# Performance work log

Hardware: AMD Instinct MI355X
Metric: run time of the kernel (lower is better)

Reference implementation:

```python
import jax, jax.numpy as jnp
import numpy as np

B, CH, H, W = 1, 128, 160, 224


def _lrelu(x):
    return jax.nn.leaky_relu(x, 0.01)


def _conv(x, w, b):
    # 1x1 conv: x [B,Cin,H,W], w [Cout,Cin], b [Cout]
    return jnp.einsum('bchw,oc->bohw', x, w) + b[None, :, None, None]


def _cmul(x, inds, Wt, b):
    # CondMul: x [N,Cin], inds [N] int32, Wt [classes,Cin,Cout], b [classes,Cout]
    return jnp.einsum('ni,nio->no', x, jnp.take(Wt, inds, axis=0)) + jnp.take(b, inds, axis=0)


def _forward(x_in, bb1_w, bb1_b, bb2_w, bb2_b, bb3_w, bb3_b,
             msk1_w, msk1_b, msk2_w, msk2_b, msk3_w, msk3_b,
             c10_w, c10_b, c20_w, c20_b, c30_w, c30_b,
             c11_W, c11_b, c21_W, c21_b, c31_W, c31_b,
             c12_W, c12_b, c22_W, c22_b, c32_W, c32_b,
             r1_w, r1_b, r2_W, r2_b, r3_W, r3_b):
    Bb, C, Hh, Ww = x_in.shape
    # backbone (1x1 convs)
    x = _lrelu(_conv(x_in, bb1_w, bb1_b))
    x = _lrelu(_conv(x, bb2_w, bb2_b))
    feat = _lrelu(_conv(x, bb3_w, bb3_b))  # [B,128,H,W]
    # mask head (note: torch applies leaky_relu to msk3 output too)
    m = _lrelu(_conv(x_in, msk1_w, msk1_b))
    m = _lrelu(_conv(m, msk2_w, msk2_b))
    mask = _lrelu(_conv(m, msk3_w, msk3_b))  # [B,1,H,W]
    # stage 1: dense classification over classes[0]=16
    y = _lrelu(_conv(feat, c10_w, c10_b))
    y = _lrelu(_conv(y, c20_w, c20_b))
    y = _conv(y, c30_w, c30_b)  # [B,16,H,W], no relu
    inds1 = jnp.argmax(y, axis=1).reshape(-1).astype(jnp.int32)  # [N], (b,h,w) order
    x_l = jnp.transpose(feat, (0, 2, 3, 1)).reshape(-1, feat.shape[1])  # [N,128]
    # stage 2: CondMul routed by inds1 (16 classes), out = 16+2*8 = 32
    t = _lrelu(_cmul(x_l, inds1, c11_W, c11_b))
    t = _lrelu(_cmul(t, inds1, c21_W, c21_b))
    t = _cmul(t, inds1, c31_W, c31_b)
    inds2 = jnp.argmax(t, axis=1).astype(jnp.int32)
    inds12 = jnp.clip(inds1 * 16 + (inds2 - 8), 0, 255).astype(jnp.int32)
    # stage 3: CondMul routed by inds12 (256 classes)
    t = _lrelu(_cmul(x_l, inds12, c12_W, c12_b))
    t = _lrelu(_cmul(t, inds12, c22_W, c22_b))
    t = _cmul(t, inds12, c32_W, c32_b)
    inds3 = jnp.argmax(t, axis=1).astype(jnp.int32)
    inds123 = jnp.clip(inds12 * 16 + (inds3 - 8), 0, 4095).astype(jnp.int32)  # classes123-1
    inds_super = inds123 // 512  # class_factor = 4096/8
    xr = _lrelu(_conv(x_in, r1_w, r1_b))
    xr_l = jnp.transpose(xr, (0, 2, 3, 1)).reshape(-1, xr.shape[1])  # [N,128]
    t = _lrelu(_cmul(xr_l, inds_super, r2_W, r2_b))
    r = _cmul(t, inds123, r3_W, r3_b).reshape(-1)
    out = ((inds123.astype(jnp.float32) + r) * (1.0 / 4096.0)).reshape(Bb, 1, Hh, Ww)
    return out, mask


def setup_inputs():
    ks = jax.random.split(jax.random.key(0), 40)
    ctr = iter(range(40))

    def p(shape, scale=0.05):
        return jax.random.normal(ks[next(ctr)], shape, dtype=jnp.float32) * scale

    d = {
        'x_in': p((B, CH, H, W), 1.0),
        'bb1_w': p((128, 128)), 'bb1_b': p((128,)),
        'bb2_w': p((128, 128)), 'bb2_b': p((128,)),
        'bb3_w': p((128, 128)), 'bb3_b': p((128,)),
        'msk1_w': p((32, 128)), 'msk1_b': p((32,)),
        'msk2_w': p((16, 32)), 'msk2_b': p((16,)),
        'msk3_w': p((1, 16)), 'msk3_b': p((1,)),
        'c10_w': p((32, 128)), 'c10_b': p((32,)),
        'c20_w': p((32, 32)), 'c20_b': p((32,)),
        'c30_w': p((16, 32)), 'c30_b': p((16,)),
        'c11_W': p((16, 128, 32)), 'c11_b': p((16, 32)),
        'c21_W': p((16, 32, 32)), 'c21_b': p((16, 32)),
        'c31_W': p((16, 32, 32)), 'c31_b': p((16, 32)),
        'c12_W': p((256, 128, 32)), 'c12_b': p((256, 32)),
        'c22_W': p((256, 32, 32)), 'c22_b': p((256, 32)),
        'c32_W': p((256, 32, 32)), 'c32_b': p((256, 32)),
        'r1_w': p((128, 128)), 'r1_b': p((128,)),
        'r2_W': p((8, 128, 32)), 'r2_b': p((8, 32)),
        'r3_W': p((4096, 32, 1)), 'r3_b': p((4096, 1)),
    }
    return d


def reference(x_in, bb1_w, bb1_b, bb2_w, bb2_b, bb3_w, bb3_b,
              msk1_w, msk1_b, msk2_w, msk2_b, msk3_w, msk3_b,
              c10_w, c10_b, c20_w, c20_b, c30_w, c30_b,
              c11_W, c11_b, c21_W, c21_b, c31_W, c31_b,
              c12_W, c12_b, c22_W, c22_b, c32_W, c32_b,
              r1_w, r1_b, r2_W, r2_b, r3_W, r3_b):
    return _forward(x_in, bb1_w, bb1_b, bb2_w, bb2_b, bb3_w, bb3_b,
                    msk1_w, msk1_b, msk2_w, msk2_b, msk3_w, msk3_b,
                    c10_w, c10_b, c20_w, c20_b, c30_w, c30_b,
                    c11_W, c11_b, c21_W, c21_b, c31_W, c31_b,
                    c12_W, c12_b, c22_W, c22_b, c32_W, c32_b,
                    r1_w, r1_b, r2_W, r2_b, r3_W, r3_b)
```

## Files before the change

### kernel.cpp

```cpp
#include <hip/hip_runtime.h>

#define N_PIX (160*224)
#define ORDER_CAP (396*256)
#define CHUNK_CAP 512
#define G_S2 156
#define G_S3 396
#define G_RG 148
#define NB   70
#define BCHUNK 512

__device__ __forceinline__ float lrelu(float v) { return v >= 0.f ? v : 0.01f * v; }

template<int CHW>
__global__ __launch_bounds__(256) void dense128_k(const float* __restrict__ in,
    const float* __restrict__ W, const float* __restrict__ b,
    float* __restrict__ out, int N)
{
  __shared__ float Wl[128*128];
  const int tid = threadIdx.x;
#pragma unroll
  for (int k = 0; k < 16; ++k)
    ((float4*)Wl)[k*256 + tid] = ((const float4*)W)[k*256 + tid];
  const int lane = tid & 63;
  const int t = tid >> 6;
  const int p = blockIdx.x * 64 + lane;
  float acc[32];
#pragma unroll
  for (int o = 0; o < 32; ++o) acc[o] = b[t*32 + o];
  __syncthreads();
  const float* xin = CHW ? (in + p) : (in + (size_t)p * 128);
  for (int c0 = 0; c0 < 128; c0 += 8) {
    float xs[8];
    if (CHW) {
#pragma unroll
      for (int k = 0; k < 8; ++k) xs[k] = xin[(size_t)(c0 + k) * N];
    } else {
      float4 xa = *(const float4*)(xin + c0);
      float4 xb = *(const float4*)(xin + c0 + 4);
      xs[0]=xa.x; xs[1]=xa.y; xs[2]=xa.z; xs[3]=xa.w;
      xs[4]=xb.x; xs[5]=xb.y; xs[6]=xb.z; xs[7]=xb.w;
    }
#pragma unroll
    for (int o = 0; o < 32; ++o) {
      const float* wr = &Wl[(t*32 + o)*128 + c0];
      float4 w0 = *(const float4*)wr;
      float4 w1 = *(const float4*)(wr + 4);
      acc[o] += xs[0]*w0.x + xs[1]*w0.y + xs[2]*w0.z + xs[3]*w0.w
              + xs[4]*w1.x + xs[5]*w1.y + xs[6]*w1.z + xs[7]*w1.w;
    }
  }
  __syncthreads();
  float4* orow = (float4*)(out + (size_t)p * 128 + t*32);
#pragma unroll
  for (int o4 = 0; o4 < 8; ++o4)
    orow[o4] = make_float4(lrelu(acc[4*o4+0]), lrelu(acc[4*o4+1]),
                           lrelu(acc[4*o4+2]), lrelu(acc[4*o4+3]));
}

__global__ __launch_bounds__(256) void mask_k(const float* __restrict__ xg,
    const float* __restrict__ W1, const float* __restrict__ b1,
    const float* __restrict__ W2, const float* __restrict__ b2,
    const float* __restrict__ W3, const float* __restrict__ b3,
    float* __restrict__ outm, int N)
{
  __shared__ float W1l[32*128], W2l[16*32], W3l[16];
  const int tid = threadIdx.x;
#pragma unroll
  for (int k = 0; k < 4; ++k)
    ((float4*)W1l)[k*256 + tid] = ((const float4*)W1)[k*256 + tid];
  if (tid < 128) ((float4*)W2l)[tid] = ((const float4*)W2)[tid];
  if (tid < 4)   ((float4*)W3l)[tid] = ((const float4*)W3)[tid];
  __syncthreads();
  const int p = blockIdx.x * 256 + tid;
  float a1[32];
#pragma unroll
  for (int o = 0; o < 32; ++o) a1[o] = b1[o];
  for (int c0 = 0; c0 < 128; c0 += 8) {
    float xs[8];
#pragma unroll
    for (int k = 0; k < 8; ++k) xs[k] = xg[(size_t)(c0 + k) * N + p];
#pragma unroll
    for (int o = 0; o < 32; ++o) {
      const float* wr = &W1l[o*128 + c0];
      float4 w0 = *(const float4*)wr, w1 = *(const float4*)(wr + 4);
      a1[o] += xs[0]*w0.x + xs[1]*w0.y + xs[2]*w0.z + xs[3]*w0.w
             + xs[4]*w1.x + xs[5]*w1.y + xs[6]*w1.z + xs[7]*w1.w;
    }
  }
#pragma unroll
  for (int o = 0; o < 32; ++o) a1[o] = lrelu(a1[o]);
  float a2[16];
#pragma unroll
  for (int o = 0; o < 16; ++o) a2[o] = b2[o];
#pragma unroll
  for (int i = 0; i < 32; i += 4) {
#pragma unroll
    for (int o = 0; o < 16; ++o) {
      float4 w = *(const float4*)&W2l[o*32 + i];
      a2[o] += a1[i]*w.x + a1[i+1]*w.y + a1[i+2]*w.z + a1[i+3]*w.w;
    }
  }
#pragma unroll
  for (int o = 0; o < 16; ++o) a2[o] = lrelu(a2[o]);
  float a3 = b3[0];
#pragma unroll
  for (int i = 0; i < 16; i += 4) {
    float4 w = *(const float4*)&W3l[i];
    a3 += a2[i]*w.x + a2[i+1]*w.y + a2[i+2]*w.z + a2[i+3]*w.w;
  }
  outm[p] = lrelu(a3);
}

__global__ __launch_bounds__(256) void stage1_k(const float* __restrict__ feat,
    const float* __restrict__ W1, const float* __restrict__ b1,
    const float* __restrict__ W2, const float* __restrict__ b2,
    const float* __restrict__ W3, const float* __restrict__ b3,
    int* __restrict__ inds1, int N)
{
  __shared__ float W1l[32*128], W2l[32*32], W3l[16*32];
  const int tid = threadIdx.x;
#pragma unroll
  for (int k = 0; k < 4; ++k)
    ((float4*)W1l)[k*256 + tid] = ((const float4*)W1)[k*256 + tid];
  ((float4*)W2l)[tid] = ((const float4*)W2)[tid];
  if (tid < 128) ((float4*)W3l)[tid] = ((const float4*)W3)[tid];
  __syncthreads();
  const int p = blockIdx.x * 256 + tid;
  const float* x = feat + (size_t)p * 128;
  float a1[32];
#pragma unroll
  for (int o = 0; o < 32; ++o) a1[o] = b1[o];
  for (int c0 = 0; c0 < 128; c0 += 8) {
    float4 xa = *(const float4*)(x + c0);
    float4 xb = *(const float4*)(x + c0 + 4);
    float xs[8] = {xa.x, xa.y, xa.z, xa.w, xb.x, xb.y, xb.z, xb.w};
#pragma unroll
    for (int o = 0; o < 32; ++o) {
      const float* wr = &W1l[o*128 + c0];
      float4 w0 = *(const float4*)wr, w1 = *(const float4*)(wr + 4);
      a1[o] += xs[0]*w0.x + xs[1]*w0.y + xs[2]*w0.z + xs[3]*w0.w
             + xs[4]*w1.x + xs[5]*w1.y + xs[6]*w1.z + xs[7]*w1.w;
    }
  }
#pragma unroll
  for (int o = 0; o < 32; ++o) a1[o] = lrelu(a1[o]);
  float a2[32];
#pragma unroll
  for (int o = 0; o < 32; ++o) a2[o] = b2[o];
#pragma unroll
  for (int i = 0; i < 32; i += 4) {
#pragma unroll
    for (int o = 0; o < 32; ++o) {
      float4 w = *(const float4*)&W2l[o*32 + i];
      a2[o] += a1[i]*w.x + a1[i+1]*w.y + a1[i+2]*w.z + a1[i+3]*w.w;
    }
  }
#pragma unroll
  for (int o = 0; o < 32; ++o) a2[o] = lrelu(a2[o]);
  float lg[16];
#pragma unroll
  for (int o = 0; o < 16; ++o) lg[o] = b3[o];
#pragma unroll
  for (int i = 0; i < 32; i += 4) {
#pragma unroll
    for (int o = 0; o < 16; ++o) {
      float4 w = *(const float4*)&W3l[o*32 + i];
      lg[o] += a2[i]*w.x + a2[i+1]*w.y + a2[i+2]*w.z + a2[i+3]*w.w;
    }
  }
  float bv = lg[0]; int bi = 0;
#pragma unroll
  for (int o = 1; o < 16; ++o) if (lg[o] > bv) { bv = lg[o]; bi = o; }
  inds1[p] = bi;
}

__global__ __launch_bounds__(256) void stage23_k(const float* __restrict__ act,
    const float* __restrict__ W1g, const float* __restrict__ b1g,
    const float* __restrict__ W2g, const float* __restrict__ b2g,
    const float* __restrict__ W3g, const float* __restrict__ b3g,
    const int* __restrict__ chunk_class, const int* __restrict__ order,
    const int* __restrict__ offs_this, const int* __restrict__ cnts_this,
    int* __restrict__ out_ind, int hi)
{
  const int cls = chunk_class[blockIdx.x];
  if (cls < 0) return;
  __shared__ float W1l[128*32], W2l[32*32], W3l[32*32];
  __shared__ float b1l[32], b2l[32], b3l[32];
  const int tid = threadIdx.x;
  const float* W1 = W1g + (size_t)cls * 4096;
  const float* W2 = W2g + (size_t)cls * 1024;
  const float* W3 = W3g + (size_t)cls * 1024;
#pragma unroll
  for (int k = 0; k < 4; ++k)
    ((float4*)W1l)[k*256 + tid] = ((const float4*)W1)[k*256 + tid];
  ((float4*)W2l)[tid] = ((const float4*)W2)[tid];
  ((float4*)W3l)[tid] = ((const float4*)W3)[tid];
  if (tid < 32) {
    b1l[tid] = b1g[cls*32 + tid];
    b2l[tid] = b2g[cls*32 + tid];
    b3l[tid] = b3g[cls*32 + tid];
  }
  const int slot = blockIdx.x * 256 + tid;
  const int end = offs_this[cls] + cnts_this[cls];
  __syncthreads();
  if (slot >= end) return;
  const int p = order[slot];
  const float* x = act + (size_t)p * 128;
  float a1[32];
#pragma unroll
  for (int o = 0; o < 32; ++o) a1[o] = b1l[o];
  for (int i0 = 0; i0 < 128; i0 += 8) {
    float4 xa = *(const float4*)(x + i0);
    float4 xb = *(const float4*)(x + i0 + 4);
    float xs[8] = {xa.x, xa.y, xa.z, xa.w, xb.x, xb.y, xb.z, xb.w};
#pragma unroll
    for (int i = 0; i < 8; ++i) {
#pragma unroll
      for (int o4 = 0; o4 < 8; ++o4) {
        float4 w = *(const float4*)&W1l[(i0 + i)*32 + o4*4];
        a1[o4*4+0] += xs[i]*w.x; a1[o4*4+1] += xs[i]*w.y;
        a1[o4*4+2] += xs[i]*w.z; a1[o4*4+3] += xs[i]*w.w;
      }
    }
  }
#pragma unroll
  for (int o = 0; o < 32; ++o) a1[o] = lrelu(a1[o]);
  float a2[32];
#pragma unroll
  for (int o = 0; o < 32; ++o) a2[o] = b2l[o];
#pragma unroll
  for (int i = 0; i < 32; ++i) {
#pragma unroll
    for (int o4 = 0; o4 < 8; ++o4) {
      float4 w = *(const float4*)&W2l[i*32 + o4*4];
      a2[o4*4+0] += a1[i]*w.x; a2[o4*4+1] += a1[i]*w.y;
      a2[o4*4+2] += a1[i]*w.z; a2[o4*4+3] += a1[i]*w.w;
    }
  }
#pragma unroll
  for (int o = 0; o < 32; ++o) a2[o] = lrelu(a2[o]);
  float a3[32];
#pragma unroll
  for (int o = 0; o < 32; ++o) a3[o] = b3l[o];
#pragma unroll
  for (int i = 0; i < 32; ++i) {
#pragma unroll
    for (int o4 = 0; o4 < 8; ++o4) {
      float4 w = *(const float4*)&W3l[i*32 + o4*4];
      a3[o4*4+0] += a2[i]*w.x; a3[o4*4+1] += a2[i]*w.y;
      a3[o4*4+2] += a2[i]*w.z; a3[o4*4+3] += a2[i]*w.w;
    }
  }
  float bv = a3[0]; int bi = 0;
#pragma unroll
  for (int o = 1; o < 32; ++o) if (a3[o] > bv) { bv = a3[o]; bi = o; }
  int v = cls*16 + bi - 8;
  v = v < 0 ? 0 : (v > hi ? hi : v);
  out_ind[p] = v;
}

__global__ __launch_bounds__(256) void reg_k(const float* __restrict__ act,
    const float* __restrict__ W1g, const float* __restrict__ b1g,
    const float* __restrict__ r3W, const float* __restrict__ r3b,
    const int* __restrict__ chunk_class, const int* __restrict__ order,
    const int* __restrict__ offs_this, const int* __restrict__ cnts_this,
    const int* __restrict__ inds123, float* __restrict__ outr)
{
  const int cls = chunk_class[blockIdx.x];
  if (cls < 0) return;
  __shared__ float W1l[128*32], b1l[32];
  const int tid = threadIdx.x;
  const float* W1 = W1g + (size_t)cls * 4096;
#pragma unroll
  for (int k = 0; k < 4; ++k)
    ((float4*)W1l)[k*256 + tid] = ((const float4*)W1)[k*256 + tid];
  if (tid < 32) b1l[tid] = b1g[cls*32 + tid];
  const int slot = blockIdx.x * 256 + tid;
  const int end = offs_this[cls] + cnts_this[cls];
  __syncthreads();
  if (slot >= end) return;
  const int p = order[slot];
  const float* x = act + (size_t)p * 128;
  float a1[32];
#pragma unroll
  for (int o = 0; o < 32; ++o) a1[o] = b1l[o];
  for (int i0 = 0; i0 < 128; i0 += 8) {
    float4 xa = *(const float4*)(x + i0);
    float4 xb = *(const float4*)(x + i0 + 4);
    float xs[8] = {xa.x, xa.y, xa.z, xa.w, xb.x, xb.y, xb.z, xb.w};
#pragma unroll
    for (int i = 0; i < 8; ++i) {
#pragma unroll
      for (int o4 = 0; o4 < 8; ++o4) {
        float4 w = *(const float4*)&W1l[(i0 + i)*32 + o4*4];
        a1[o4*4+0] += xs[i]*w.x; a1[o4*4+1] += xs[i]*w.y;
        a1[o4*4+2] += xs[i]*w.z; a1[o4*4+3] += xs[i]*w.w;
      }
    }
  }
#pragma unroll
  for (int o = 0; o < 32; ++o) a1[o] = lrelu(a1[o]);
  const int ind = inds123[p];
  const float4* rw = (const float4*)(r3W + (size_t)ind * 32);
  float r = r3b[ind];
#pragma unroll
  for (int k = 0; k < 8; ++k) {
    float4 w = rw[k];
    r += a1[4*k+0]*w.x + a1[4*k+1]*w.y + a1[4*k+2]*w.z + a1[4*k+3]*w.w;
  }
  outr[p] = ((float)ind + r) * (1.0f / 4096.0f);
}

__global__ __launch_bounds__(256) void hist_k(const int* __restrict__ ind,
    int* __restrict__ blkcnt, int shift, int C)
{
  __shared__ int h[256];
  const int tid = threadIdx.x, b = blockIdx.x;
  h[tid] = 0;
  __syncthreads();
  const int base = b * BCHUNK;
  atomicAdd(&h[ind[base + tid] >> shift], 1);
  atomicAdd(&h[ind[base + 256 + tid] >> shift], 1);
  __syncthreads();
  if (tid < C) blkcnt[b * C + tid] = h[tid];
}

__global__ __launch_bounds__(256) void scan_k(const int* __restrict__ blkcnt,
    int* __restrict__ blkbase, int* __restrict__ offsets, int* __restrict__ counts,
    int* __restrict__ chunk_class, int C, int fillTo)
{
  __shared__ int cl[256], ol[256];
  __shared__ int totChunks;
  const int tid = threadIdx.x;
  if (tid < C) {
    int s = 0;
    for (int b = 0; b < NB; ++b) s += blkcnt[b * C + tid];
    cl[tid] = s;
  }
  __syncthreads();
  if (tid == 0) {
    int off = 0;
    for (int c = 0; c < C; ++c) {
      ol[c] = off;
      off += ((cl[c] + 255) >> 8) << 8;
    }
    totChunks = off >> 8;
  }
  __syncthreads();
  if (tid < C) {
    offsets[tid] = ol[tid];
    counts[tid]  = cl[tid];
    int acc = ol[tid];
    for (int b = 0; b < NB; ++b) {
      int v = blkcnt[b * C + tid];
      blkbase[b * C + tid] = acc;
      acc += v;
    }
    const int start = ol[tid] >> 8;
    const int nch = (cl[tid] + 255) >> 8;
    for (int k = 0; k < nch; ++k) chunk_class[start + k] = tid;
  }
  for (int k = totChunks + tid; k < fillTo; k += 256) chunk_class[k] = -1;
}

__global__ __launch_bounds__(256) void scatter_k(const int* __restrict__ ind,
    const int* __restrict__ blkbase, int* __restrict__ order, int shift, int C)
{
  __shared__ int lcur[256], lbase[256];
  const int tid = threadIdx.x, b = blockIdx.x;
  lcur[tid] = 0;
  if (tid < C) lbase[tid] = blkbase[b * C + tid];
  __syncthreads();
  const int base = b * BCHUNK;
#pragma unroll
  for (int r = 0; r < BCHUNK; r += 256) {
    const int p = base + r + tid;
    const int c = ind[p] >> shift;
    const int rank = atomicAdd(&lcur[c], 1);
    order[lbase[c] + rank] = p;
  }
}

extern "C" void kernel_launch(void* const* d_in, const int* in_sizes, int n_in,
                              void* d_out, int out_size, void* d_ws, size_t ws_size,
                              hipStream_t stream)
{
  const int N = N_PIX;
  const float* x_in  = (const float*)d_in[0];
  const float* bb1_w = (const float*)d_in[1];  const float* bb1_b = (const float*)d_in[2];
  const float* bb2_w = (const float*)d_in[3];  const float* bb2_b = (const float*)d_in[4];
  const float* bb3_w = (const float*)d_in[5];  const float* bb3_b = (const float*)d_in[6];
  const float* msk1_w= (const float*)d_in[7];  const float* msk1_b= (const float*)d_in[8];
  const float* msk2_w= (const float*)d_in[9];  const float* msk2_b= (const float*)d_in[10];
  const float* msk3_w= (const float*)d_in[11]; const float* msk3_b= (const float*)d_in[12];
  const float* c10_w = (const float*)d_in[13]; const float* c10_b = (const float*)d_in[14];
  const float* c20_w = (const float*)d_in[15]; const float* c20_b = (const float*)d_in[16];
  const float* c30_w = (const float*)d_in[17]; const float* c30_b = (const float*)d_in[18];
  const float* c11_W = (const float*)d_in[19]; const float* c11_b = (const float*)d_in[20];
  const float* c21_W = (const float*)d_in[21]; const float* c21_b = (const float*)d_in[22];
  const float* c31_W = (const float*)d_in[23]; const float* c31_b = (const float*)d_in[24];
  const float* c12_W = (const float*)d_in[25]; const float* c12_b = (const float*)d_in[26];
  const float* c22_W = (const float*)d_in[27]; const float* c22_b = (const float*)d_in[28];
  const float* c32_W = (const float*)d_in[29]; const float* c32_b = (const float*)d_in[30];
  const float* r1_w  = (const float*)d_in[31]; const float* r1_b  = (const float*)d_in[32];
  const float* r2_W  = (const float*)d_in[33]; const float* r2_b  = (const float*)d_in[34];
  const float* r3_W  = (const float*)d_in[35]; const float* r3_b  = (const float*)d_in[36];

  float* act     = (float*)d_ws;
  int*   inds1   = (int*)(act + (size_t)N * 128);
  int*   inds12  = inds1 + N;
  int*   inds123 = inds12 + N;
  int*   counts  = inds123 + N;
  int*   offs    = counts + 256;
  int*   chunk_cls = offs + 256;
  int*   order     = chunk_cls + CHUNK_CAP;
  int*   blkcnt    = order + ORDER_CAP;
  int*   blkbase   = blkcnt + NB*256;

  float* out_reg  = (float*)d_out;
  float* out_mask = out_reg + N;

  const dim3 B(256);
  const int gPix64  = N / 64;
  const int gPix256 = N / 256;

  dense128_k<1><<<gPix64, B, 0, stream>>>(x_in, bb1_w, bb1_b, act, N);
  dense128_k<0><<<gPix64, B, 0, stream>>>(act,  bb2_w, bb2_b, act, N);
  dense128_k<0><<<gPix64, B, 0, stream>>>(act,  bb3_w, bb3_b, act, N);

  mask_k<<<gPix256, B, 0, stream>>>(x_in, msk1_w, msk1_b, msk2_w, msk2_b,
                                    msk3_w, msk3_b, out_mask, N);

  stage1_k<<<gPix256, B, 0, stream>>>(act, c10_w, c10_b, c20_w, c20_b,
                                      c30_w, c30_b, inds1, N);

  hist_k<<<NB, B, 0, stream>>>(inds1, blkcnt, 0, 16);
  scan_k<<<1, B, 0, stream>>>(blkcnt, blkbase, offs, counts, chunk_cls, 16, G_S2);
  scatter_k<<<NB, B, 0, stream>>>(inds1, blkbase, order, 0, 16);
  stage23_k<<<G_S2, B, 0, stream>>>(act, c11_W, c11_b, c21_W, c21_b, c31_W, c31_b,
                                    chunk_cls, order, offs, counts, inds12, 255);

  hist_k<<<NB, B, 0, stream>>>(inds12, blkcnt, 0, 256);
  scan_k<<<1, B, 0, stream>>>(blkcnt, blkbase, offs, counts, chunk_cls, 256, G_S3);
  scatter_k<<<NB, B, 0, stream>>>(inds12, blkbase, order, 0, 256);
  stage23_k<<<G_S3, B, 0, stream>>>(act, c12_W, c12_b, c22_W, c22_b, c32_W, c32_b,
                                    chunk_cls, order, offs, counts, inds123, 4095);

  dense128_k<1><<<gPix64, B, 0, stream>>>(x_in, r1_w, r1_b, act, N);

  hist_k<<<NB, B, 0, stream>>>(inds123, blkcnt, 9, 8);
  scan_k<<<1, B, 0, stream>>>(blkcnt, blkbase, offs, counts, chunk_cls, 8, G_RG);
  scatter_k<<<NB, B, 0, stream>>>(inds123, blkbase, order, 9, 8);
  reg_k<<<G_RG, B, 0, stream>>>(act, r2_W, r2_b, r3_W, r3_b,
                                chunk_cls, order, offs, counts, inds123, out_reg);
}
```

Baseline: 526.3 us.

## Retile dense128 to two pixels per thread and fuse stage-1 histogram

The dense 1x1 conv kernel now runs 512-thread blocks covering 128 pixels. Each thread computes 16 outputs for two pixels, so every shared-memory weight load is reused twice and the LDS traffic per FMA is halved. Separately, stage1 builds the per-block class histogram with shared atomics and writes blkcnt directly. This removes one hist_k launch and its re-read of inds1. Scan and scatter take a block count and chunk size so they can consume the 140 blocks of 256 pixels, at the cost of extra atomics in stage1.

After: 533.4 us. Within noise of the previous version (+1.3%).

```diff
diff --git a/kernel.cpp b/kernel.cpp
--- a/kernel.cpp
+++ b/kernel.cpp
@@ -12,49 +12,63 @@
 __device__ __forceinline__ float lrelu(float v) { return v >= 0.f ? v : 0.01f * v; }
 
 template<int CHW>
-__global__ __launch_bounds__(256) void dense128_k(const float* __restrict__ in,
+__global__ __launch_bounds__(512) void dense128_k(const float* __restrict__ in,
     const float* __restrict__ W, const float* __restrict__ b,
     float* __restrict__ out, int N)
 {
   __shared__ float Wl[128*128];
   const int tid = threadIdx.x;
 #pragma unroll
-  for (int k = 0; k < 16; ++k)
-    ((float4*)Wl)[k*256 + tid] = ((const float4*)W)[k*256 + tid];
+  for (int k = 0; k < 8; ++k)
+    ((float4*)Wl)[k*512 + tid] = ((const float4*)W)[k*512 + tid];
   const int lane = tid & 63;
-  const int t = tid >> 6;
-  const int p = blockIdx.x * 64 + lane;
-  float acc[32];
-#pragma unroll
-  for (int o = 0; o < 32; ++o) acc[o] = b[t*32 + o];
-  __syncthreads();
-  const float* xin = CHW ? (in + p) : (in + (size_t)p * 128);
+  const int wv = tid >> 6;
+  const int ob = wv * 16;
+  const int p0 = blockIdx.x * 128 + lane;
+  const int p1 = p0 + 64;
+  float acc0[16], acc1[16];
+#pragma unroll
+  for (int o = 0; o < 16; ++o) { acc0[o] = b[ob + o]; acc1[o] = acc0[o]; }
+  __syncthreads();
+  const float* x0 = CHW ? (in + p0) : (in + (size_t)p0 * 128);
+  const float* x1 = CHW ? (in + p1) : (in + (size_t)p1 * 128);
   for (int c0 = 0; c0 < 128; c0 += 8) {
-    float xs[8];
+    float xa[8], xb[8];
     if (CHW) {
 #pragma unroll
-      for (int k = 0; k < 8; ++k) xs[k] = xin[(size_t)(c0 + k) * N];
+      for (int k = 0; k < 8; ++k) {
+        xa[k] = x0[(size_t)(c0 + k) * N];
+        xb[k] = x1[(size_t)(c0 + k) * N];
+      }
     } else {
-      float4 xa = *(const float4*)(xin + c0);
-      float4 xb = *(const float4*)(xin + c0 + 4);
-      xs[0]=xa.x; xs[1]=xa.y; xs[2]=xa.z; xs[3]=xa.w;
-      xs[4]=xb.x; xs[5]=xb.y; xs[6]=xb.z; xs[7]=xb.w;
-    }
-#pragma unroll
-    for (int o = 0; o < 32; ++o) {
-      const float* wr = &Wl[(t*32 + o)*128 + c0];
+      float4 a0 = *(const float4*)(x0 + c0), a1 = *(const float4*)(x0 + c0 + 4);
+      float4 b0 = *(const float4*)(x1 + c0), b1 = *(const float4*)(x1 + c0 + 4);
+      xa[0]=a0.x; xa[1]=a0.y; xa[2]=a0.z; xa[3]=a0.w;
+      xa[4]=a1.x; xa[5]=a1.y; xa[6]=a1.z; xa[7]=a1.w;
+      xb[0]=b0.x; xb[1]=b0.y; xb[2]=b0.z; xb[3]=b0.w;
+      xb[4]=b1.x; xb[5]=b1.y; xb[6]=b1.z; xb[7]=b1.w;
+    }
+#pragma unroll
+    for (int o = 0; o < 16; ++o) {
+      const float* wr = &Wl[(ob + o)*128 + c0];
       float4 w0 = *(const float4*)wr;
       float4 w1 = *(const float4*)(wr + 4);
-      acc[o] += xs[0]*w0.x + xs[1]*w0.y + xs[2]*w0.z + xs[3]*w0.w
-              + xs[4]*w1.x + xs[5]*w1.y + xs[6]*w1.z + xs[7]*w1.w;
-    }
-  }
-  __syncthreads();
-  float4* orow = (float4*)(out + (size_t)p * 128 + t*32);
-#pragma unroll
-  for (int o4 = 0; o4 < 8; ++o4)
-    orow[o4] = make_float4(lrelu(acc[4*o4+0]), lrelu(acc[4*o4+1]),
-                           lrelu(acc[4*o4+2]), lrelu(acc[4*o4+3]));
+      acc0[o] += xa[0]*w0.x + xa[1]*w0.y + xa[2]*w0.z + xa[3]*w0.w
+               + xa[4]*w1.x + xa[5]*w1.y + xa[6]*w1.z + xa[7]*w1.w;
+      acc1[o] += xb[0]*w0.x + xb[1]*w0.y + xb[2]*w0.z + xb[3]*w0.w
+               + xb[4]*w1.x + xb[5]*w1.y + xb[6]*w1.z + xb[7]*w1.w;
+    }
+  }
+  __syncthreads();
+  float4* o0 = (float4*)(out + (size_t)p0 * 128 + ob);
+  float4* o1 = (float4*)(out + (size_t)p1 * 128 + ob);
+#pragma unroll
+  for (int q = 0; q < 4; ++q) {
+    o0[q] = make_float4(lrelu(acc0[4*q+0]), lrelu(acc0[4*q+1]),
+                        lrelu(acc0[4*q+2]), lrelu(acc0[4*q+3]));
+    o1[q] = make_float4(lrelu(acc1[4*q+0]), lrelu(acc1[4*q+1]),
+                        lrelu(acc1[4*q+2]), lrelu(acc1[4*q+3]));
+  }
 }
 
 __global__ __launch_bounds__(256) void mask_k(const float* __restrict__ xg,
@@ -115,15 +129,17 @@
     const float* __restrict__ W1, const float* __restrict__ b1,
     const float* __restrict__ W2, const float* __restrict__ b2,
     const float* __restrict__ W3, const float* __restrict__ b3,
-    int* __restrict__ inds1, int N)
+    int* __restrict__ inds1, int* __restrict__ blkcnt, int N)
 {
   __shared__ float W1l[32*128], W2l[32*32], W3l[16*32];
+  __shared__ int hist[16];
   const int tid = threadIdx.x;
 #pragma unroll
   for (int k = 0; k < 4; ++k)
     ((float4*)W1l)[k*256 + tid] = ((const float4*)W1)[k*256 + tid];
   ((float4*)W2l)[tid] = ((const float4*)W2)[tid];
   if (tid < 128) ((float4*)W3l)[tid] = ((const float4*)W3)[tid];
+  if (tid < 16) hist[tid] = 0;
   __syncthreads();
   const int p = blockIdx.x * 256 + tid;
   const float* x = feat + (size_t)p * 128;
@@ -172,6 +188,9 @@
 #pragma unroll
   for (int o = 1; o < 16; ++o) if (lg[o] > bv) { bv = lg[o]; bi = o; }
   inds1[p] = bi;
+  atomicAdd(&hist[bi], 1);
+  __syncthreads();
+  if (tid < 16) blkcnt[blockIdx.x * 16 + tid] = hist[tid];
 }
 
 __global__ __launch_bounds__(256) void stage23_k(const float* __restrict__ act,
@@ -327,14 +346,14 @@
 
 __global__ __launch_bounds__(256) void scan_k(const int* __restrict__ blkcnt,
     int* __restrict__ blkbase, int* __restrict__ offsets, int* __restrict__ counts,
-    int* __restrict__ chunk_class, int C, int fillTo)
+    int* __restrict__ chunk_class, int C, int fillTo, int nb)
 {
   __shared__ int cl[256], ol[256];
   __shared__ int totChunks;
   const int tid = threadIdx.x;
   if (tid < C) {
     int s = 0;
-    for (int b = 0; b < NB; ++b) s += blkcnt[b * C + tid];
+    for (int b = 0; b < nb; ++b) s += blkcnt[b * C + tid];
     cl[tid] = s;
   }
   __syncthreads();
@@ -351,7 +370,7 @@
     offsets[tid] = ol[tid];
     counts[tid]  = cl[tid];
     int acc = ol[tid];
-    for (int b = 0; b < NB; ++b) {
+    for (int b = 0; b < nb; ++b) {
       int v = blkcnt[b * C + tid];
       blkbase[b * C + tid] = acc;
       acc += v;
@@ -364,16 +383,16 @@
 }
 
 __global__ __launch_bounds__(256) void scatter_k(const int* __restrict__ ind,
-    const int* __restrict__ blkbase, int* __restrict__ order, int shift, int C)
+    const int* __restrict__ blkbase, int* __restrict__ order, int shift, int C,
+    int chunkpx)
 {
   __shared__ int lcur[256], lbase[256];
   const int tid = threadIdx.x, b = blockIdx.x;
   lcur[tid] = 0;
   if (tid < C) lbase[tid] = blkbase[b * C + tid];
   __syncthreads();
-  const int base = b * BCHUNK;
-#pragma unroll
-  for (int r = 0; r < BCHUNK; r += 256) {
+  const int base = b * chunkpx;
+  for (int r = 0; r < chunkpx; r += 256) {
     const int p = base + r + tid;
     const int c = ind[p] >> shift;
     const int rank = atomicAdd(&lcur[c], 1);
@@ -415,42 +434,42 @@
   int*   chunk_cls = offs + 256;
   int*   order     = chunk_cls + CHUNK_CAP;
   int*   blkcnt    = order + ORDER_CAP;
-  int*   blkbase   = blkcnt + NB*256;
+  int*   blkbase   = blkcnt + 70*256;
 
   float* out_reg  = (float*)d_out;
   float* out_mask = out_reg + N;
 
   const dim3 B(256);
-  const int gPix64  = N / 64;
+  const dim3 B512(512);
+  const int gDense  = N / 128;
   const int gPix256 = N / 256;
 
-  dense128_k<1><<<gPix64, B, 0, stream>>>(x_in, bb1_w, bb1_b, act, N);
-  dense128_k<0><<<gPix64, B, 0, stream>>>(act,  bb2_w, bb2_b, act, N);
-  dense128_k<0><<<gPix64, B, 0, stream>>>(act,  bb3_w, bb3_b, act, N);
+  dense128_k<1><<<gDense, B512, 0, stream>>>(x_in, bb1_w, bb1_b, act, N);
+  dense128_k<0><<<gDense, B512, 0, stream>>>(act,  bb2_w, bb2_b, act, N);
+  dense128_k<0><<<gDense, B512, 0, stream>>>(act,  bb3_w, bb3_b, act, N);
 
   mask_k<<<gPix256, B, 0, stream>>>(x_in, msk1_w, msk1_b, msk2_w, msk2_b,
                                     msk3_w, msk3_b, out_mask, N);
 
   stage1_k<<<gPix256, B, 0, stream>>>(act, c10_w, c10_b, c20_w, c20_b,
-                                      c30_w, c30_b, inds1, N);
-
-  hist_k<<<NB, B, 0, stream>>>(inds1, blkcnt, 0, 16);
-  scan_k<<<1, B, 0, stream>>>(blkcnt, blkbase, offs, counts, chunk_cls, 16, G_S2);
-  scatter_k<<<NB, B, 0, stream>>>(inds1, blkbase, order, 0, 16);
+                                      c30_w, c30_b, inds1, blkcnt, N);
+
+  scan_k<<<1, B, 0, stream>>>(blkcnt, blkbase, offs, counts, chunk_cls, 16, G_S2, 140);
+  scatter_k<<<140, B, 0, stream>>>(inds1, blkbase, order, 0, 16, 256);
   stage23_k<<<G_S2, B, 0, stream>>>(act, c11_W, c11_b, c21_W, c21_b, c31_W, c31_b,
                                     chunk_cls, order, offs, counts, inds12, 255);
 
   hist_k<<<NB, B, 0, stream>>>(inds12, blkcnt, 0, 256);
-  scan_k<<<1, B, 0, stream>>>(blkcnt, blkbase, offs, counts, chunk_cls, 256, G_S3);
-  scatter_k<<<NB, B, 0, stream>>>(inds12, blkbase, order, 0, 256);
+  scan_k<<<1, B, 0, stream>>>(blkcnt, blkbase, offs, counts, chunk_cls, 256, G_S3, NB);
+  scatter_k<<<NB, B, 0, stream>>>(inds12, blkbase, order, 0, 256, BCHUNK);
   stage23_k<<<G_S3, B, 0, stream>>>(act, c12_W, c12_b, c22_W, c22_b, c32_W, c32_b,
                                     chunk_cls, order, offs, counts, inds123, 4095);
 
-  dense128_k<1><<<gPix64, B, 0, stream>>>(x_in, r1_w, r1_b, act, N);
+  dense128_k<1><<<gDense, B512, 0, stream>>>(x_in, r1_w, r1_b, act, N);
 
   hist_k<<<NB, B, 0, stream>>>(inds123, blkcnt, 9, 8);
-  scan_k<<<1, B, 0, stream>>>(blkcnt, blkbase, offs, counts, chunk_cls, 8, G_RG);
-  scatter_k<<<NB, B, 0, stream>>>(inds123, blkbase, order, 9, 8);
+  scan_k<<<1, B, 0, stream>>>(blkcnt, blkbase, offs, counts, chunk_cls, 8, G_RG, NB);
+  scatter_k<<<NB, B, 0, stream>>>(inds123, blkbase, order, 9, 8, BCHUNK);
   reg_k<<<G_RG, B, 0, stream>>>(act, r2_W, r2_b, r3_W, r3_b,
                                 chunk_cls, order, offs, counts, inds123, out_reg);
 }
```
